# Performance work log

Measured on AMD Instinct MI355X. Metric: run time of the kernel, lower is better.

Reference implementation:

```python
import jax, jax.numpy as jnp
import numpy as np

V = 50257   # output_vocab_size
H = 1024    # hidden_size_gru
E = 1024    # embedding_size (must equal H for d_i = transform(h)+g to typecheck)
L = 20      # max sentence length (cnn feature length)


def setup_inputs() -> dict:
    key = jax.random.key(0)
    ks = jax.random.split(key, 16)
    s = 0.02
    return {
        "y_i": jax.random.randint(ks[0], (1, 1), 0, V),
        "h_i": jax.random.normal(ks[1], (1, 1, H), jnp.float32),
        "cnn_a": jax.random.normal(ks[2], (1, E, L), jnp.float32),
        "cnn_c": jax.random.normal(ks[3], (1, E, L), jnp.float32),
        "emb": jax.random.normal(ks[4], (V, H), jnp.float32) * s,
        "W_t": jax.random.normal(ks[5], (E, H), jnp.float32) * s,
        "b_t": jnp.zeros((E,), jnp.float32),
        "W_ih": jax.random.normal(ks[6], (3 * H, H + E), jnp.float32) * s,
        "W_hh": jax.random.normal(ks[7], (3 * H, H), jnp.float32) * s,
        "b_ih": jnp.zeros((3 * H,), jnp.float32),
        "b_hh": jnp.zeros((3 * H,), jnp.float32),
        "W_o": jax.random.normal(ks[8], (V, H), jnp.float32) * s,
        "b_o": jnp.zeros((V,), jnp.float32),
    }


def reference(y_i, h_i, cnn_a, cnn_c, emb, W_t, b_t, W_ih, W_hh, b_ih, b_hh, W_o, b_o):
    # embedding lookup (dropout is identity in eval / p=0)
    g_i = emb[y_i]                                         # [1,1,H]
    # attention query: transform_gru_hidden(h_i) + g_i
    d_i = jnp.einsum('bth,eh->bte', h_i, W_t) + b_t + g_i  # [1,1,E]
    scores = jnp.einsum('bte,bel->btl', d_i, cnn_a).reshape(1, -1)  # [1,L]
    a_i = jax.nn.softmax(scores, axis=-1)                  # [1,L]
    # context: bmm(a, cnn_c^T)
    c_i = jnp.einsum('bl,bel->be', a_i, cnn_c)[:, None, :]  # [1,1,E]
    # single-step GRU (PyTorch gate layout: r, z, n)
    x = jnp.concatenate([g_i, c_i], axis=-1)[0]            # [1, H+E]
    h = h_i[0]                                             # [1, H]
    gi = x @ W_ih.T + b_ih                                 # [1, 3H]
    gh = h @ W_hh.T + b_hh                                 # [1, 3H]
    ir, iz, in_ = jnp.split(gi, 3, axis=-1)
    hr, hz, hn = jnp.split(gh, 3, axis=-1)
    r = jax.nn.sigmoid(ir + hr)
    z = jax.nn.sigmoid(iz + hz)
    n = jnp.tanh(in_ + r * hn)
    h_new = (1.0 - z) * n + z * h                          # [1, H]
    gru_hidden = h_new[None]                               # [1,1,H]
    logits = h_new @ W_o.T + b_o                           # [1, V]
    softmax_output = jax.nn.log_softmax(logits, axis=-1)
    return softmax_output, gru_hidden
```

## Files before the change

kernel.cpp:

```cpp
#include <hip/hip_runtime.h>


#define V_SIZE 50257
#define HDIM   1024
#define LDIM   20

__device__ __forceinline__ float wave_sum(float v) {
#pragma unroll
    for (int o = 32; o > 0; o >>= 1) v += __shfl_down(v, o, 64);
    return v;
}

__global__ void __launch_bounds__(256)
k_dvec(const float* __restrict__ Wt, const float* __restrict__ bt,
       const float* __restrict__ hvec, const float* __restrict__ emb,
       const int* __restrict__ y, float* __restrict__ dvec) {
    int e = blockIdx.x, t = threadIdx.x;
    float4 w  = ((const float4*)(Wt + (size_t)e * HDIM))[t];
    float4 hh = ((const float4*)hvec)[t];
    float s = w.x*hh.x + w.y*hh.y + w.z*hh.z + w.w*hh.w;
    s = wave_sum(s);
    __shared__ float part[4];
    if ((t & 63) == 0) part[t >> 6] = s;
    __syncthreads();
    if (t == 0) {
        float tot = part[0] + part[1] + part[2] + part[3];
        int yy = y[0];
        tot += bt[e] + emb[(size_t)yy * HDIM + e];
        dvec[e] = tot;
    }
}

__global__ void __launch_bounds__(1024)
k_attn(const float* __restrict__ dvec, const float* __restrict__ cnn_a,
       const float* __restrict__ cnn_c, float* __restrict__ cvec) {
    int t = threadIdx.x;
    float d = dvec[t];
    float p[LDIM];
    const float* ar = cnn_a + t * LDIM;
#pragma unroll
    for (int l = 0; l < LDIM; ++l) p[l] = d * ar[l];
#pragma unroll
    for (int l = 0; l < LDIM; ++l) p[l] = wave_sum(p[l]);
    __shared__ float part[16 * LDIM];
    int w = t >> 6;
    if ((t & 63) == 0) {
#pragma unroll
        for (int l = 0; l < LDIM; ++l) part[w * LDIM + l] = p[l];
    }
    __syncthreads();
    __shared__ float aw[LDIM];
    if (t == 0) {
        float sc[LDIM];
        for (int l = 0; l < LDIM; ++l) {
            float s = 0.f;
            for (int w2 = 0; w2 < 16; ++w2) s += part[w2 * LDIM + l];
            sc[l] = s;
        }
        float m = sc[0];
        for (int l = 1; l < LDIM; ++l) m = fmaxf(m, sc[l]);
        float ss = 0.f;
        for (int l = 0; l < LDIM; ++l) { sc[l] = expf(sc[l] - m); ss += sc[l]; }
        float inv = 1.0f / ss;
        for (int l = 0; l < LDIM; ++l) aw[l] = sc[l] * inv;
    }
    __syncthreads();
    const float* cr = cnn_c + t * LDIM;
    float c = 0.f;
#pragma unroll
    for (int l = 0; l < LDIM; ++l) c += aw[l] * cr[l];
    cvec[t] = c;
}

__global__ void __launch_bounds__(256)
k_gru(const float* __restrict__ Wih, const float* __restrict__ Whh,
      const float* __restrict__ bih, const float* __restrict__ bhh,
      const float* __restrict__ hvec, const float* __restrict__ emb,
      const int* __restrict__ y, const float* __restrict__ cvec,
      float* __restrict__ hnew, float* __restrict__ out_h) {
    int j = blockIdx.x, t = threadIdx.x;
    int base = t * 8;
    float xs[8];
    const float* xsrc;
    if (t < 128) {
        int yy = y[0];
        xsrc = emb + (size_t)yy * HDIM + base;
    } else {
        xsrc = cvec + (base - 1024);
    }
    {
        float4 a = ((const float4*)xsrc)[0], b = ((const float4*)xsrc)[1];
        xs[0]=a.x; xs[1]=a.y; xs[2]=a.z; xs[3]=a.w;
        xs[4]=b.x; xs[5]=b.y; xs[6]=b.z; xs[7]=b.w;
    }
    float4 hq = ((const float4*)hvec)[t];

    float acc[6];
#pragma unroll
    for (int g = 0; g < 3; ++g) {
        const float* wr = Wih + (size_t)(j + g * 1024) * 2048 + base;
        float4 a = ((const float4*)wr)[0], b = ((const float4*)wr)[1];
        acc[g] = a.x*xs[0] + a.y*xs[1] + a.z*xs[2] + a.w*xs[3]
               + b.x*xs[4] + b.y*xs[5] + b.z*xs[6] + b.w*xs[7];
    }
#pragma unroll
    for (int g = 0; g < 3; ++g) {
        float4 q = ((const float4*)(Whh + (size_t)(j + g * 1024) * 1024))[t];
        acc[3 + g] = q.x*hq.x + q.y*hq.y + q.z*hq.z + q.w*hq.w;
    }
    __shared__ float part[4][6];
#pragma unroll
    for (int i = 0; i < 6; ++i) {
        float s = wave_sum(acc[i]);
        if ((t & 63) == 0) part[t >> 6][i] = s;
    }
    __syncthreads();
    if (t == 0) {
        float v[6];
#pragma unroll
        for (int i = 0; i < 6; ++i) v[i] = part[0][i] + part[1][i] + part[2][i] + part[3][i];
        float ir  = v[0] + bih[j];
        float iz  = v[1] + bih[j + 1024];
        float in_ = v[2] + bih[j + 2048];
        float hr  = v[3] + bhh[j];
        float hz  = v[4] + bhh[j + 1024];
        float hn  = v[5] + bhh[j + 2048];
        float r = 1.0f / (1.0f + expf(-(ir + hr)));
        float z = 1.0f / (1.0f + expf(-(iz + hz)));
        float n = tanhf(in_ + r * hn);
        float hj = hvec[j];
        float hv = (1.0f - z) * n + z * hj;
        hnew[j] = hv;
        out_h[j] = hv;
    }
}

__global__ void __launch_bounds__(256)
k_logits(const float* __restrict__ Wo, const float* __restrict__ bo,
         const float* __restrict__ hnew, float* __restrict__ logits,
         float* __restrict__ pm, float* __restrict__ ps) {
    int t = threadIdx.x;
    int lane = t & 63, w = t >> 6;
    int wave_id = blockIdx.x * 4 + w;
    int nwaves = gridDim.x * 4;
    float h[16];
    const float4* hv4 = (const float4*)hnew;
#pragma unroll
    for (int i = 0; i < 4; ++i) {
        float4 q = hv4[lane * 4 + i];
        h[i*4+0]=q.x; h[i*4+1]=q.y; h[i*4+2]=q.z; h[i*4+3]=q.w;
    }
    float m = -1e30f, s = 0.0f;
    for (int v = wave_id; v < V_SIZE; v += nwaves) {
        const float4* row = (const float4*)(Wo + (size_t)v * HDIM);
        float4 q0 = row[lane*4+0], q1 = row[lane*4+1], q2 = row[lane*4+2], q3 = row[lane*4+3];
        float a = q0.x*h[0]  + q0.y*h[1]  + q0.z*h[2]  + q0.w*h[3]
                + q1.x*h[4]  + q1.y*h[5]  + q1.z*h[6]  + q1.w*h[7]
                + q2.x*h[8]  + q2.y*h[9]  + q2.z*h[10] + q2.w*h[11]
                + q3.x*h[12] + q3.y*h[13] + q3.z*h[14] + q3.w*h[15];
        a = wave_sum(a);
        if (lane == 0) {
            float lv = a + bo[v];
            logits[v] = lv;
            float mn = fmaxf(m, lv);
            s = s * expf(m - mn) + expf(lv - mn);
            m = mn;
        }
    }
    if (lane == 0) { pm[wave_id] = m; ps[wave_id] = s; }
}

__global__ void __launch_bounds__(256)
k_out(const float* __restrict__ logits, const float* __restrict__ pm,
      const float* __restrict__ ps, float* __restrict__ out, int nwaves) {
    int t = threadIdx.x;
    float m = -1e30f, s = 0.0f;
    for (int i = t; i < nwaves; i += 256) {
        float m2 = pm[i], s2 = ps[i];
        float mn = fmaxf(m, m2);
        s = s * expf(m - mn) + s2 * expf(m2 - mn);
        m = mn;
    }
#pragma unroll
    for (int o = 32; o > 0; o >>= 1) {
        float m2 = __shfl_down(m, o, 64);
        float s2 = __shfl_down(s, o, 64);
        float mn = fmaxf(m, m2);
        s = s * expf(m - mn) + s2 * expf(m2 - mn);
        m = mn;
    }
    __shared__ float sm[4], ssv[4];
    if ((t & 63) == 0) { sm[t >> 6] = m; ssv[t >> 6] = s; }
    __syncthreads();
    __shared__ float logZ;
    if (t == 0) {
        float M = sm[0], S = ssv[0];
        for (int i = 1; i < 4; ++i) {
            float mn = fmaxf(M, sm[i]);
            S = S * expf(M - mn) + ssv[i] * expf(sm[i] - mn);
            M = mn;
        }
        logZ = M + logf(S);
    }
    __syncthreads();
    float lz = logZ;
    for (int v = blockIdx.x * 256 + t; v < V_SIZE; v += gridDim.x * 256)
        out[v] = logits[v] - lz;
}

extern "C" void kernel_launch(void* const* d_in, const int* in_sizes, int n_in,
                              void* d_out, int out_size, void* d_ws, size_t ws_size,
                              hipStream_t stream) {
    const int*   y     = (const int*)d_in[0];
    const float* h_i   = (const float*)d_in[1];
    const float* cnn_a = (const float*)d_in[2];
    const float* cnn_c = (const float*)d_in[3];
    const float* emb   = (const float*)d_in[4];
    const float* W_t   = (const float*)d_in[5];
    const float* b_t   = (const float*)d_in[6];
    const float* W_ih  = (const float*)d_in[7];
    const float* W_hh  = (const float*)d_in[8];
    const float* b_ih  = (const float*)d_in[9];
    const float* b_hh  = (const float*)d_in[10];
    const float* W_o   = (const float*)d_in[11];
    const float* b_o   = (const float*)d_in[12];
    float*       out   = (float*)d_out;

    float* ws     = (float*)d_ws;
    float* dvec   = ws;
    float* cvec   = ws + 1024;
    float* hnew   = ws + 2048;
    float* logits = ws + 4096;
    float* pm     = ws + 54528;
    float* ps     = ws + 58624;

    k_dvec<<<1024, 256, 0, stream>>>(W_t, b_t, h_i, emb, y, dvec);
    k_attn<<<1, 1024, 0, stream>>>(dvec, cnn_a, cnn_c, cvec);
    k_gru<<<1024, 256, 0, stream>>>(W_ih, W_hh, b_ih, b_hh, h_i, emb, y, cvec,
                                    hnew, out + V_SIZE);
    k_logits<<<1024, 256, 0, stream>>>(W_o, b_o, hnew, logits, pm, ps);
    k_out<<<256, 256, 0, stream>>>(logits, pm, ps, out, 1024 * 4);
}
```

Baseline: 427.9 us.

## Fuse attention into GRU blocks and process two vocab rows per wave

New measurement: 427.0 us. About the same (-0.2%).

```diff
diff --git a/kernel.cpp b/kernel.cpp
--- a/kernel.cpp
+++ b/kernel.cpp
@@ -31,32 +31,38 @@
     }
 }
 
-__global__ void __launch_bounds__(1024)
-k_attn(const float* __restrict__ dvec, const float* __restrict__ cnn_a,
-       const float* __restrict__ cnn_c, float* __restrict__ cvec) {
-    int t = threadIdx.x;
-    float d = dvec[t];
+__global__ void __launch_bounds__(256)
+k_gru(const float* __restrict__ Wih, const float* __restrict__ Whh,
+      const float* __restrict__ bih, const float* __restrict__ bhh,
+      const float* __restrict__ hvec, const float* __restrict__ emb,
+      const int* __restrict__ y, const float* __restrict__ dvec,
+      const float* __restrict__ cnn_a, const float* __restrict__ cnn_c,
+      float* __restrict__ hnew, float* __restrict__ out_h) {
+    int j = blockIdx.x, t = threadIdx.x;
+
     float p[LDIM];
-    const float* ar = cnn_a + t * LDIM;
-#pragma unroll
-    for (int l = 0; l < LDIM; ++l) p[l] = d * ar[l];
+    {
+        float4 d4 = ((const float4*)dvec)[t];
+        const float* ar = cnn_a + (size_t)t * 4 * LDIM;
+#pragma unroll
+        for (int l = 0; l < LDIM; ++l)
+            p[l] = d4.x * ar[l] + d4.y * ar[LDIM + l]
+                 + d4.z * ar[2 * LDIM + l] + d4.w * ar[3 * LDIM + l];
+    }
 #pragma unroll
     for (int l = 0; l < LDIM; ++l) p[l] = wave_sum(p[l]);
-    __shared__ float part[16 * LDIM];
-    int w = t >> 6;
+    __shared__ float spart[4 * LDIM];
     if ((t & 63) == 0) {
-#pragma unroll
-        for (int l = 0; l < LDIM; ++l) part[w * LDIM + l] = p[l];
+        int w = t >> 6;
+#pragma unroll
+        for (int l = 0; l < LDIM; ++l) spart[w * LDIM + l] = p[l];
     }
     __syncthreads();
     __shared__ float aw[LDIM];
     if (t == 0) {
         float sc[LDIM];
-        for (int l = 0; l < LDIM; ++l) {
-            float s = 0.f;
-            for (int w2 = 0; w2 < 16; ++w2) s += part[w2 * LDIM + l];
-            sc[l] = s;
-        }
+        for (int l = 0; l < LDIM; ++l)
+            sc[l] = spart[l] + spart[LDIM + l] + spart[2 * LDIM + l] + spart[3 * LDIM + l];
         float m = sc[0];
         for (int l = 1; l < LDIM; ++l) m = fmaxf(m, sc[l]);
         float ss = 0.f;
@@ -65,33 +71,35 @@
         for (int l = 0; l < LDIM; ++l) aw[l] = sc[l] * inv;
     }
     __syncthreads();
-    const float* cr = cnn_c + t * LDIM;
-    float c = 0.f;
-#pragma unroll
-    for (int l = 0; l < LDIM; ++l) c += aw[l] * cr[l];
-    cvec[t] = c;
-}
-
-__global__ void __launch_bounds__(256)
-k_gru(const float* __restrict__ Wih, const float* __restrict__ Whh,
-      const float* __restrict__ bih, const float* __restrict__ bhh,
-      const float* __restrict__ hvec, const float* __restrict__ emb,
-      const int* __restrict__ y, const float* __restrict__ cvec,
-      float* __restrict__ hnew, float* __restrict__ out_h) {
-    int j = blockIdx.x, t = threadIdx.x;
+    __shared__ float csh[1024];
+    {
+        const float* cr = cnn_c + (size_t)t * 4 * LDIM;
+        float c0 = 0.f, c1 = 0.f, c2 = 0.f, c3 = 0.f;
+#pragma unroll
+        for (int l = 0; l < LDIM; ++l) {
+            float a = aw[l];
+            c0 += a * cr[l];
+            c1 += a * cr[LDIM + l];
+            c2 += a * cr[2 * LDIM + l];
+            c3 += a * cr[3 * LDIM + l];
+        }
+        csh[4 * t + 0] = c0; csh[4 * t + 1] = c1;
+        csh[4 * t + 2] = c2; csh[4 * t + 3] = c3;
+    }
+    __syncthreads();
+
     int base = t * 8;
     float xs[8];
-    const float* xsrc;
     if (t < 128) {
         int yy = y[0];
-        xsrc = emb + (size_t)yy * HDIM + base;
-    } else {
-        xsrc = cvec + (base - 1024);
-    }
-    {
+        const float* xsrc = emb + (size_t)yy * HDIM + base;
         float4 a = ((const float4*)xsrc)[0], b = ((const float4*)xsrc)[1];
         xs[0]=a.x; xs[1]=a.y; xs[2]=a.z; xs[3]=a.w;
         xs[4]=b.x; xs[5]=b.y; xs[6]=b.z; xs[7]=b.w;
+    } else {
+        int cb = base - 1024;
+#pragma unroll
+        for (int i = 0; i < 8; ++i) xs[i] = csh[cb + i];
     }
     float4 hq = ((const float4*)hvec)[t];
 
@@ -142,7 +150,7 @@
     int t = threadIdx.x;
     int lane = t & 63, w = t >> 6;
     int wave_id = blockIdx.x * 4 + w;
-    int nwaves = gridDim.x * 4;
+    const int nwaves = 4096;
     float h[16];
     const float4* hv4 = (const float4*)hnew;
 #pragma unroll
@@ -151,31 +159,62 @@
         h[i*4+0]=q.x; h[i*4+1]=q.y; h[i*4+2]=q.z; h[i*4+3]=q.w;
     }
     float m = -1e30f, s = 0.0f;
-    for (int v = wave_id; v < V_SIZE; v += nwaves) {
-        const float4* row = (const float4*)(Wo + (size_t)v * HDIM);
-        float4 q0 = row[lane*4+0], q1 = row[lane*4+1], q2 = row[lane*4+2], q3 = row[lane*4+3];
+    for (int v0 = wave_id * 2; v0 < V_SIZE; v0 += 2 * nwaves) {
+        const float4* rA = (const float4*)(Wo + (size_t)v0 * HDIM);
+        float4 q0 = rA[lane*4+0], q1 = rA[lane*4+1], q2 = rA[lane*4+2], q3 = rA[lane*4+3];
         float a = q0.x*h[0]  + q0.y*h[1]  + q0.z*h[2]  + q0.w*h[3]
                 + q1.x*h[4]  + q1.y*h[5]  + q1.z*h[6]  + q1.w*h[7]
                 + q2.x*h[8]  + q2.y*h[9]  + q2.z*h[10] + q2.w*h[11]
                 + q3.x*h[12] + q3.y*h[13] + q3.z*h[14] + q3.w*h[15];
+        int v1 = v0 + 1;
+        bool hasB = (v1 < V_SIZE);
+        float b = 0.0f;
+        if (hasB) {
+            const float4* rB = (const float4*)(Wo + (size_t)v1 * HDIM);
+            float4 r0 = rB[lane*4+0], r1 = rB[lane*4+1], r2 = rB[lane*4+2], r3 = rB[lane*4+3];
+            b = r0.x*h[0]  + r0.y*h[1]  + r0.z*h[2]  + r0.w*h[3]
+              + r1.x*h[4]  + r1.y*h[5]  + r1.z*h[6]  + r1.w*h[7]
+              + r2.x*h[8]  + r2.y*h[9]  + r2.z*h[10] + r2.w*h[11]
+              + r3.x*h[12] + r3.y*h[13] + r3.z*h[14] + r3.w*h[15];
+        }
         a = wave_sum(a);
+        b = wave_sum(b);
         if (lane == 0) {
-            float lv = a + bo[v];
-            logits[v] = lv;
+            float lv = a + bo[v0];
+            logits[v0] = lv;
             float mn = fmaxf(m, lv);
             s = s * expf(m - mn) + expf(lv - mn);
             m = mn;
-        }
-    }
-    if (lane == 0) { pm[wave_id] = m; ps[wave_id] = s; }
+            if (hasB) {
+                float lv1 = b + bo[v1];
+                logits[v1] = lv1;
+                float mn1 = fmaxf(m, lv1);
+                s = s * expf(m - mn1) + expf(lv1 - mn1);
+                m = mn1;
+            }
+        }
+    }
+    __shared__ float sm[4], ssv[4];
+    if (lane == 0) { sm[w] = m; ssv[w] = s; }
+    __syncthreads();
+    if (t == 0) {
+        float M = sm[0], S = ssv[0];
+#pragma unroll
+        for (int i = 1; i < 4; ++i) {
+            float mn = fmaxf(M, sm[i]);
+            S = S * expf(M - mn) + ssv[i] * expf(sm[i] - mn);
+            M = mn;
+        }
+        pm[blockIdx.x] = M; ps[blockIdx.x] = S;
+    }
 }
 
 __global__ void __launch_bounds__(256)
 k_out(const float* __restrict__ logits, const float* __restrict__ pm,
-      const float* __restrict__ ps, float* __restrict__ out, int nwaves) {
+      const float* __restrict__ ps, float* __restrict__ out, int nparts) {
     int t = threadIdx.x;
     float m = -1e30f, s = 0.0f;
-    for (int i = t; i < nwaves; i += 256) {
+    for (int i = t; i < nparts; i += 256) {
         float m2 = pm[i], s2 = ps[i];
         float mn = fmaxf(m, m2);
         s = s * expf(m - mn) + s2 * expf(m2 - mn);
@@ -228,16 +267,14 @@
 
     float* ws     = (float*)d_ws;
     float* dvec   = ws;
-    float* cvec   = ws + 1024;
     float* hnew   = ws + 2048;
     float* logits = ws + 4096;
     float* pm     = ws + 54528;
     float* ps     = ws + 58624;
 
     k_dvec<<<1024, 256, 0, stream>>>(W_t, b_t, h_i, emb, y, dvec);
-    k_attn<<<1, 1024, 0, stream>>>(dvec, cnn_a, cnn_c, cvec);
-    k_gru<<<1024, 256, 0, stream>>>(W_ih, W_hh, b_ih, b_hh, h_i, emb, y, cvec,
-                                    hnew, out + V_SIZE);
+    k_gru<<<1024, 256, 0, stream>>>(W_ih, W_hh, b_ih, b_hh, h_i, emb, y, dvec,
+                                    cnn_a, cnn_c, hnew, out + V_SIZE);
     k_logits<<<1024, 256, 0, stream>>>(W_o, b_o, hnew, logits, pm, ps);
-    k_out<<<256, 256, 0, stream>>>(logits, pm, ps, out, 1024 * 4);
-}
+    k_out<<<256, 256, 0, stream>>>(logits, pm, ps, out, 1024);
+}
```
